# Kernel tuning notes

Hardware: AMD Instinct MI355X
Metric: run time of the kernel (lower is better)

Reference implementation:

```python
import jax, jax.numpy as jnp
import numpy as np
from jax import lax

VOCAB_SIZE = 13
E = 13          # embedding_dim == len(VOCAB)
H = 1024        # weights_dim (LSTM hidden)
HL = 512        # hidden_layer_dim (MLP)
OUT = 2
T = 16384       # sequence length


def setup_inputs() -> dict:
    key = jax.random.key(0)
    ks = jax.random.split(key, 12)
    s_ih = 1.0 / np.sqrt(H)  # PyTorch LSTMCell default init scale
    inp = {
        "x": jax.random.normal(ks[0], (T, E), dtype=jnp.float32),
        "h0": jax.random.normal(ks[1], (1, H), dtype=jnp.float32) * np.sqrt(2.0 / (1 + H)),
        "c0": jax.random.normal(ks[2], (1, H), dtype=jnp.float32) * np.sqrt(2.0 / (1 + H)),
        "W_ih": jax.random.uniform(ks[3], (4 * H, E), jnp.float32, -s_ih, s_ih),
        "W_hh": jax.random.uniform(ks[4], (4 * H, H), jnp.float32, -s_ih, s_ih),
        "b_ih": jax.random.uniform(ks[5], (4 * H,), jnp.float32, -s_ih, s_ih),
        "b_hh": jax.random.uniform(ks[6], (4 * H,), jnp.float32, -s_ih, s_ih),
        "W1": jax.random.uniform(ks[7], (HL, H), jnp.float32, -1.0 / np.sqrt(H), 1.0 / np.sqrt(H)),
        "b1": jax.random.uniform(ks[8], (HL,), jnp.float32, -1.0 / np.sqrt(H), 1.0 / np.sqrt(H)),
        "W2": jax.random.uniform(ks[9], (OUT, HL), jnp.float32, -1.0 / np.sqrt(HL), 1.0 / np.sqrt(HL)),
        "b2": jax.random.uniform(ks[10], (OUT,), jnp.float32, -1.0 / np.sqrt(HL), 1.0 / np.sqrt(HL)),
    }
    return inp


def reference(x, h0, c0, W_ih, W_hh, b_ih, b_hh, W1, b1, W2, b2):
    # x: [T, E] (batch dim of the original view is 1, folded away)
    # Precompute input-to-gate projections for all timesteps (same math, one GEMM).
    xg = x @ W_ih.T + b_ih  # [T, 4H]

    def step(carry, xg_t):
        h, c = carry  # [1, H] each
        gates = xg_t + h @ W_hh.T + b_hh  # [1, 4H]
        i, f, g, o = jnp.split(gates, 4, axis=-1)
        c = jax.nn.sigmoid(f) * c + jax.nn.sigmoid(i) * jnp.tanh(g)
        h = jax.nn.sigmoid(o) * jnp.tanh(c)
        return (h, c), None

    (h, c), _ = lax.scan(step, (h0, c0), xg[:, None, :])
    out = jnp.tanh(h @ W1.T + b1) @ W2.T + b2  # [1, 2]
    return out
```

## Files before the change

kernel.cpp:

```cpp
#include <hip/hip_runtime.h>
#include <cstdint>
#include <cstddef>

#define NWG 64
#define NTHR 512
#define UPW 16
#define TSTEPS 16384
#define HDIM 1024
#define EDIM 13
#define HLDIM 512

typedef unsigned long long ull;

__global__ void k_init(const float* __restrict__ h0, ull* __restrict__ hrec,
                       ull* __restrict__ urec) {
  int i = threadIdx.x;
  hrec[i] = (ull)__float_as_uint(h0[i]);
  hrec[HDIM + i] = 0ull;
  hrec[2 * HDIM + i] = 0ull;
  hrec[3 * HDIM + i] = 0ull;
  if (i < HLDIM) urec[i] = 0ull;
}

__global__ __launch_bounds__(NTHR) void k_main(
    const float* __restrict__ x, const float* __restrict__ c0,
    const float* __restrict__ Wih, const float* __restrict__ Whh,
    const float* __restrict__ bih, const float* __restrict__ bhh,
    const float* __restrict__ W1, const float* __restrict__ b1,
    const float* __restrict__ W2, const float* __restrict__ b2,
    float* __restrict__ out, ull* hrec, ull* urec) {
  const int w = blockIdx.x;
  const int tid = threadIdx.x;
  const int wave = tid >> 6;
  const int lane = tid & 63;
  const int hi = lane >> 5;
  const int sl = lane & 31;
  const int lu = 2 * wave + hi;

  __shared__ float4 lds_w4[32 * 256];
  __shared__ float4 lds_h4[2 * 256];
  __shared__ float lds_wih[64][17];
  __shared__ float lds_bsum[64];
  __shared__ float lds_r0[8], lds_r1[8];
  __shared__ float lds_xbuf[2][16];
  float* lds_hf = (float*)lds_h4;

#pragma unroll
  for (int it = 0; it < 16; ++it) {
    int idx = it * NTHR + tid;
    int r = idx >> 8;
    int c4 = idx & 255;
    int lu_ = r >> 2, g_ = r & 3;
    int grow = g_ * HDIM + UPW * w + lu_;
    lds_w4[r * 256 + c4] = ((const float4*)(Whh + (size_t)grow * HDIM))[c4];
  }
  if (tid < 64) {
    int lu_ = tid >> 2, g_ = tid & 3;
    int grow = g_ * HDIM + UPW * w + lu_;
#pragma unroll
    for (int e = 0; e < EDIM; ++e) lds_wih[tid][e] = Wih[grow * EDIM + e];
    lds_bsum[tid] = bih[grow] + bhh[grow];
  }
  float cst = c0[UPW * w + lu];
  __syncthreads();

  const int myg = sl & 3;
  const float gsc = (myg == 2) ? 2.f : 1.f;
  const float4* wl0 = lds_w4 + (size_t)(4 * lu + 0) * 256;
  const float4* wl1 = lds_w4 + (size_t)(4 * lu + 1) * 256;
  const float4* wl2 = lds_w4 + (size_t)(4 * lu + 2) * 256;
  const float4* wl3 = lds_w4 + (size_t)(4 * lu + 3) * 256;
  const float4* gg0 =
      (const float4*)(Whh + (size_t)(0 * HDIM + UPW * w + lu) * HDIM);
  const float4* gg1 =
      (const float4*)(Whh + (size_t)(1 * HDIM + UPW * w + lu) * HDIM);
  const float4* gg2 =
      (const float4*)(Whh + (size_t)(2 * HDIM + UPW * w + lu) * HDIM);
  const float4* gg3 =
      (const float4*)(Whh + (size_t)(3 * HDIM + UPW * w + lu) * HDIM);

  for (int t = 1; t <= TSTEPS; ++t) {
    const int lp = (t - 1) & 1;

    if (wave == 0) {
      float xv = 0.f;
      if (lane < EDIM) xv = x[(size_t)(t - 1) * EDIM + lane];

      const ull* src = hrec + (size_t)((t - 1) & 3) * HDIM;
      const unsigned want = (unsigned)(t - 1);
      ull v0, v1, v2, v3, v4, v5, v6, v7, v8, v9, va, vb, vc, vd, ve, vf;
      for (;;) {
        v0 = __hip_atomic_load(&src[lane], __ATOMIC_RELAXED,
                               __HIP_MEMORY_SCOPE_AGENT);
        v1 = __hip_atomic_load(&src[lane + 64], __ATOMIC_RELAXED,
                               __HIP_MEMORY_SCOPE_AGENT);
        v2 = __hip_atomic_load(&src[lane + 128], __ATOMIC_RELAXED,
                               __HIP_MEMORY_SCOPE_AGENT);
        v3 = __hip_atomic_load(&src[lane + 192], __ATOMIC_RELAXED,
                               __HIP_MEMORY_SCOPE_AGENT);
        v4 = __hip_atomic_load(&src[lane + 256], __ATOMIC_RELAXED,
                               __HIP_MEMORY_SCOPE_AGENT);
        v5 = __hip_atomic_load(&src[lane + 320], __ATOMIC_RELAXED,
                               __HIP_MEMORY_SCOPE_AGENT);
        v6 = __hip_atomic_load(&src[lane + 384], __ATOMIC_RELAXED,
                               __HIP_MEMORY_SCOPE_AGENT);
        v7 = __hip_atomic_load(&src[lane + 448], __ATOMIC_RELAXED,
                               __HIP_MEMORY_SCOPE_AGENT);
        v8 = __hip_atomic_load(&src[lane + 512], __ATOMIC_RELAXED,
                               __HIP_MEMORY_SCOPE_AGENT);
        v9 = __hip_atomic_load(&src[lane + 576], __ATOMIC_RELAXED,
                               __HIP_MEMORY_SCOPE_AGENT);
        va = __hip_atomic_load(&src[lane + 640], __ATOMIC_RELAXED,
                               __HIP_MEMORY_SCOPE_AGENT);
        vb = __hip_atomic_load(&src[lane + 704], __ATOMIC_RELAXED,
                               __HIP_MEMORY_SCOPE_AGENT);
        vc = __hip_atomic_load(&src[lane + 768], __ATOMIC_RELAXED,
                               __HIP_MEMORY_SCOPE_AGENT);
        vd = __hip_atomic_load(&src[lane + 832], __ATOMIC_RELAXED,
                               __HIP_MEMORY_SCOPE_AGENT);
        ve = __hip_atomic_load(&src[lane + 896], __ATOMIC_RELAXED,
                               __HIP_MEMORY_SCOPE_AGENT);
        vf = __hip_atomic_load(&src[lane + 960], __ATOMIC_RELAXED,
                               __HIP_MEMORY_SCOPE_AGENT);
        unsigned ok = ((unsigned)(v0 >> 32) == want) &
                      ((unsigned)(v1 >> 32) == want) &
                      ((unsigned)(v2 >> 32) == want) &
                      ((unsigned)(v3 >> 32) == want) &
                      ((unsigned)(v4 >> 32) == want) &
                      ((unsigned)(v5 >> 32) == want) &
                      ((unsigned)(v6 >> 32) == want) &
                      ((unsigned)(v7 >> 32) == want) &
                      ((unsigned)(v8 >> 32) == want) &
                      ((unsigned)(v9 >> 32) == want) &
                      ((unsigned)(va >> 32) == want) &
                      ((unsigned)(vb >> 32) == want) &
                      ((unsigned)(vc >> 32) == want) &
                      ((unsigned)(vd >> 32) == want) &
                      ((unsigned)(ve >> 32) == want) &
                      ((unsigned)(vf >> 32) == want);
        if (ok) break;
      }
      float* dst = lds_hf + lp * HDIM + lane;
      dst[0] = __uint_as_float((unsigned)v0);
      dst[64] = __uint_as_float((unsigned)v1);
      dst[128] = __uint_as_float((unsigned)v2);
      dst[192] = __uint_as_float((unsigned)v3);
      dst[256] = __uint_as_float((unsigned)v4);
      dst[320] = __uint_as_float((unsigned)v5);
      dst[384] = __uint_as_float((unsigned)v6);
      dst[448] = __uint_as_float((unsigned)v7);
      dst[512] = __uint_as_float((unsigned)v8);
      dst[576] = __uint_as_float((unsigned)v9);
      dst[640] = __uint_as_float((unsigned)va);
      dst[704] = __uint_as_float((unsigned)vb);
      dst[768] = __uint_as_float((unsigned)vc);
      dst[832] = __uint_as_float((unsigned)vd);
      dst[896] = __uint_as_float((unsigned)ve);
      dst[960] = __uint_as_float((unsigned)vf);
      if (lane < EDIM) lds_xbuf[lp][lane] = xv;
    }
    __syncthreads();

    const float4* hb = lds_h4 + lp * 256;
    float4 hv0 = hb[sl], hv1 = hb[sl + 32], hv2 = hb[sl + 64],
           hv3 = hb[sl + 96], hv4 = hb[sl + 128], hv5 = hb[sl + 160],
           hv6 = hb[sl + 192], hv7 = hb[sl + 224];

#define ROWDOT(dst, srcp)                                               \
  {                                                                     \
    float4 a = (srcp)[sl], b = (srcp)[sl + 32], c = (srcp)[sl + 64],    \
           d = (srcp)[sl + 96], e4 = (srcp)[sl + 128],                  \
           f4 = (srcp)[sl + 160], g4 = (srcp)[sl + 192],                \
           i4 = (srcp)[sl + 224];                                       \
    dst = (a.x * hv0.x + a.y * hv0.y + a.z * hv0.z + a.w * hv0.w) +     \
          (b.x * hv1.x + b.y * hv1.y + b.z * hv1.z + b.w * hv1.w) +     \
          (c.x * hv2.x + c.y * hv2.y + c.z * hv2.z + c.w * hv2.w) +     \
          (d.x * hv3.x + d.y * hv3.y + d.z * hv3.z + d.w * hv3.w) +     \
          (e4.x * hv4.x + e4.y * hv4.y + e4.z * hv4.z + e4.w * hv4.w) + \
          (f4.x * hv5.x + f4.y * hv5.y + f4.z * hv5.z + f4.w * hv5.w) + \
          (g4.x * hv6.x + g4.y * hv6.y + g4.z * hv6.z + g4.w * hv6.w) + \
          (i4.x * hv7.x + i4.y * hv7.y + i4.z * hv7.z + i4.w * hv7.w);  \
  }

    float acc0, acc1, acc2, acc3;
    if (lu < 8) {
      ROWDOT(acc0, wl0);
      ROWDOT(acc1, wl1);
      ROWDOT(acc2, wl2);
      ROWDOT(acc3, wl3);
    } else {
      ROWDOT(acc0, gg0);
      ROWDOT(acc1, gg1);
      ROWDOT(acc2, gg2);
      ROWDOT(acc3, gg3);
    }
#undef ROWDOT

    if (sl < 4) {
      int lrow = lu * 4 + sl;
      float xd = lds_bsum[lrow];
#pragma unroll
      for (int e = 0; e < EDIM; ++e) xd += lds_wih[lrow][e] * lds_xbuf[lp][e];
      if (sl == 0) acc0 += xd;
      else if (sl == 1) acc1 += xd;
      else if (sl == 2) acc2 += xd;
      else acc3 += xd;
    }

#pragma unroll
    for (int m = 1; m < 32; m <<= 1) {
      acc0 += __shfl_xor(acc0, m);
      acc1 += __shfl_xor(acc1, m);
      acc2 += __shfl_xor(acc2, m);
      acc3 += __shfl_xor(acc3, m);
    }

    float pre = (myg == 0) ? acc0 : (myg == 1) ? acc1 : (myg == 2) ? acc2
                                                                   : acc3;
    float e = __expf(-gsc * pre);
    float y = 1.f / (1.f + e);
    float act = (myg == 2) ? 2.f * y - 1.f : y;

    int base = lane & 32;
    float ai = __shfl(act, base + 0);
    float af = __shfl(act, base + 1);
    float ag = __shfl(act, base + 2);
    float ao = __shfl(act, base + 3);
    if (sl == 0) {
      cst = af * cst + ai * ag;
      float e2 = __expf(-2.f * cst);
      float hn = ao * (2.f / (1.f + e2) - 1.f);
      ull pk = ((ull)(unsigned)t << 32) | (ull)__float_as_uint(hn);
      __hip_atomic_store(&hrec[(size_t)(t & 3) * HDIM + UPW * w + lu], pk,
                         __ATOMIC_RELAXED, __HIP_MEMORY_SCOPE_AGENT);
    }
  }

  {
    const unsigned want = (unsigned)TSTEPS;
    ull v0 = __hip_atomic_load(&hrec[tid], __ATOMIC_RELAXED,
                               __HIP_MEMORY_SCOPE_AGENT);
    ull v1 = __hip_atomic_load(&hrec[tid + NTHR], __ATOMIC_RELAXED,
                               __HIP_MEMORY_SCOPE_AGENT);
    for (;;) {
      bool b0 = (unsigned)(v0 >> 32) == want;
      bool b1 = (unsigned)(v1 >> 32) == want;
      if (b0 && b1) break;
      if (!b0)
        v0 = __hip_atomic_load(&hrec[tid], __ATOMIC_RELAXED,
                               __HIP_MEMORY_SCOPE_AGENT);
      if (!b1)
        v1 = __hip_atomic_load(&hrec[tid + NTHR], __ATOMIC_RELAXED,
                               __HIP_MEMORY_SCOPE_AGENT);
    }
    lds_hf[tid] = __uint_as_float((unsigned)v0);
    lds_hf[tid + NTHR] = __uint_as_float((unsigned)v1);
  }
  __syncthreads();
  {
    int r1 = 8 * w + wave;
    const float* w1p = W1 + (size_t)r1 * HDIM + lane * 16;
    float a0 = 0.f, a1 = 0.f;
#pragma unroll
    for (int i = 0; i < 16; i += 2) {
      a0 += w1p[i] * lds_hf[lane * 16 + i];
      a1 += w1p[i + 1] * lds_hf[lane * 16 + i + 1];
    }
    float acc1 = a0 + a1;
#pragma unroll
    for (int m = 1; m < 64; m <<= 1) acc1 += __shfl_xor(acc1, m);
    if (lane == 0) {
      float e2 = __expf(-2.f * (acc1 + b1[r1]));
      float u = 2.f / (1.f + e2) - 1.f;
      ull pk = (1ull << 32) | (ull)__float_as_uint(u);
      __hip_atomic_store(&urec[r1], pk, __ATOMIC_RELAXED,
                         __HIP_MEMORY_SCOPE_AGENT);
    }
  }

  if (w == 0) {
    ull uv = __hip_atomic_load(&urec[tid], __ATOMIC_RELAXED,
                               __HIP_MEMORY_SCOPE_AGENT);
    while ((unsigned)(uv >> 32) != 1u)
      uv = __hip_atomic_load(&urec[tid], __ATOMIC_RELAXED,
                             __HIP_MEMORY_SCOPE_AGENT);
    float u = __uint_as_float((unsigned)uv);
    float p0 = W2[tid] * u;
    float p1 = W2[HLDIM + tid] * u;
#pragma unroll
    for (int m = 1; m < 64; m <<= 1) {
      p0 += __shfl_xor(p0, m);
      p1 += __shfl_xor(p1, m);
    }
    if (lane == 0) {
      lds_r0[wave] = p0;
      lds_r1[wave] = p1;
    }
    __syncthreads();
    if (tid == 0) {
      float o0 = b2[0], o1 = b2[1];
#pragma unroll
      for (int k = 0; k < 8; ++k) {
        o0 += lds_r0[k];
        o1 += lds_r1[k];
      }
      out[0] = o0;
      out[1] = o1;
    }
  }
}

extern "C" void kernel_launch(void* const* d_in, const int* in_sizes, int n_in,
                              void* d_out, int out_size, void* d_ws,
                              size_t ws_size, hipStream_t stream) {
  const float* x = (const float*)d_in[0];
  const float* h0 = (const float*)d_in[1];
  const float* c0 = (const float*)d_in[2];
  const float* Wih = (const float*)d_in[3];
  const float* Whh = (const float*)d_in[4];
  const float* bih = (const float*)d_in[5];
  const float* bhh = (const float*)d_in[6];
  const float* W1 = (const float*)d_in[7];
  const float* b1 = (const float*)d_in[8];
  const float* W2 = (const float*)d_in[9];
  const float* b2 = (const float*)d_in[10];
  float* out = (float*)d_out;

  ull* hrec = (ull*)d_ws;
  ull* urec = (ull*)((char*)d_ws + 4 * HDIM * sizeof(ull));

  k_init<<<1, 1024, 0, stream>>>(h0, hrec, urec);
  k_main<<<NWG, NTHR, 0, stream>>>(x, c0, Wih, Whh, bih, bhh, W1, b1, W2, b2,
                                   out, hrec, urec);
}
```

Measured before the change: 56.88 ms.

## Add two dedicated loader waves with LDS ready flags replacing per-step block barrier

The block grows from 8 to 10 waves. Two producer waves take turns polling the global h records for alternating timesteps and write h and x into a 4-deep LDS ring, then publish a per-slot ready flag. The 8 compute waves spin on that LDS flag instead of a __syncthreads, so the fetch of h for step t+1 can overlap compute of step t and the block-wide barrier leaves the critical path. The cost is extra waves, 4x more LDS for h, and volatile-flag spinning whose ordering rests on an explicit lgkmcnt wait.

```diff
diff --git a/kernel.cpp b/kernel.cpp
--- a/kernel.cpp
+++ b/kernel.cpp
@@ -3,7 +3,7 @@
 #include <cstddef>
 
 #define NWG 64
-#define NTHR 512
+#define NTHR 640
 #define UPW 16
 #define TSTEPS 16384
 #define HDIM 1024
@@ -35,24 +35,28 @@
   const int lane = tid & 63;
   const int hi = lane >> 5;
   const int sl = lane & 31;
-  const int lu = 2 * wave + hi;
+  const int cwave = wave - 2;
+  const int lu = (cwave >= 0) ? 2 * cwave + hi : 0;
 
   __shared__ float4 lds_w4[32 * 256];
-  __shared__ float4 lds_h4[2 * 256];
+  __shared__ float4 lds_h4[4 * 256];
   __shared__ float lds_wih[64][17];
   __shared__ float lds_bsum[64];
+  __shared__ float lds_xbuf[4][16];
   __shared__ float lds_r0[8], lds_r1[8];
-  __shared__ float lds_xbuf[2][16];
+  __shared__ int lds_rdy[4];
   float* lds_hf = (float*)lds_h4;
 
 #pragma unroll
-  for (int it = 0; it < 16; ++it) {
+  for (int it = 0; it < 13; ++it) {
     int idx = it * NTHR + tid;
-    int r = idx >> 8;
-    int c4 = idx & 255;
-    int lu_ = r >> 2, g_ = r & 3;
-    int grow = g_ * HDIM + UPW * w + lu_;
-    lds_w4[r * 256 + c4] = ((const float4*)(Whh + (size_t)grow * HDIM))[c4];
+    if (idx < 8192) {
+      int r = idx >> 8;
+      int c4 = idx & 255;
+      int lu_ = r >> 2, g_ = r & 3;
+      int grow = g_ * HDIM + UPW * w + lu_;
+      lds_w4[r * 256 + c4] = ((const float4*)(Whh + (size_t)grow * HDIM))[c4];
+    }
   }
   if (tid < 64) {
     int lu_ = tid >> 2, g_ = tid & 3;
@@ -61,86 +65,65 @@
     for (int e = 0; e < EDIM; ++e) lds_wih[tid][e] = Wih[grow * EDIM + e];
     lds_bsum[tid] = bih[grow] + bhh[grow];
   }
-  float cst = c0[UPW * w + lu];
+  if (tid < 4) lds_rdy[tid] = -1;
+  float cst = (cwave >= 0) ? c0[UPW * w + lu] : 0.f;
   __syncthreads();
 
-  const int myg = sl & 3;
-  const float gsc = (myg == 2) ? 2.f : 1.f;
-  const float4* wl0 = lds_w4 + (size_t)(4 * lu + 0) * 256;
-  const float4* wl1 = lds_w4 + (size_t)(4 * lu + 1) * 256;
-  const float4* wl2 = lds_w4 + (size_t)(4 * lu + 2) * 256;
-  const float4* wl3 = lds_w4 + (size_t)(4 * lu + 3) * 256;
-  const float4* gg0 =
-      (const float4*)(Whh + (size_t)(0 * HDIM + UPW * w + lu) * HDIM);
-  const float4* gg1 =
-      (const float4*)(Whh + (size_t)(1 * HDIM + UPW * w + lu) * HDIM);
-  const float4* gg2 =
-      (const float4*)(Whh + (size_t)(2 * HDIM + UPW * w + lu) * HDIM);
-  const float4* gg3 =
-      (const float4*)(Whh + (size_t)(3 * HDIM + UPW * w + lu) * HDIM);
-
-  for (int t = 1; t <= TSTEPS; ++t) {
-    const int lp = (t - 1) & 1;
-
-    if (wave == 0) {
+  if (wave < 2) {
+    for (int t = 1 + wave; t <= TSTEPS; t += 2) {
+      const int p = (t - 1) & 3;
       float xv = 0.f;
       if (lane < EDIM) xv = x[(size_t)(t - 1) * EDIM + lane];
 
-      const ull* src = hrec + (size_t)((t - 1) & 3) * HDIM;
+      const ull* src = hrec + (size_t)p * HDIM + lane;
       const unsigned want = (unsigned)(t - 1);
       ull v0, v1, v2, v3, v4, v5, v6, v7, v8, v9, va, vb, vc, vd, ve, vf;
       for (;;) {
-        v0 = __hip_atomic_load(&src[lane], __ATOMIC_RELAXED,
-                               __HIP_MEMORY_SCOPE_AGENT);
-        v1 = __hip_atomic_load(&src[lane + 64], __ATOMIC_RELAXED,
-                               __HIP_MEMORY_SCOPE_AGENT);
-        v2 = __hip_atomic_load(&src[lane + 128], __ATOMIC_RELAXED,
-                               __HIP_MEMORY_SCOPE_AGENT);
-        v3 = __hip_atomic_load(&src[lane + 192], __ATOMIC_RELAXED,
-                               __HIP_MEMORY_SCOPE_AGENT);
-        v4 = __hip_atomic_load(&src[lane + 256], __ATOMIC_RELAXED,
-                               __HIP_MEMORY_SCOPE_AGENT);
-        v5 = __hip_atomic_load(&src[lane + 320], __ATOMIC_RELAXED,
-                               __HIP_MEMORY_SCOPE_AGENT);
-        v6 = __hip_atomic_load(&src[lane + 384], __ATOMIC_RELAXED,
-                               __HIP_MEMORY_SCOPE_AGENT);
-        v7 = __hip_atomic_load(&src[lane + 448], __ATOMIC_RELAXED,
-                               __HIP_MEMORY_SCOPE_AGENT);
-        v8 = __hip_atomic_load(&src[lane + 512], __ATOMIC_RELAXED,
-                               __HIP_MEMORY_SCOPE_AGENT);
-        v9 = __hip_atomic_load(&src[lane + 576], __ATOMIC_RELAXED,
-                               __HIP_MEMORY_SCOPE_AGENT);
-        va = __hip_atomic_load(&src[lane + 640], __ATOMIC_RELAXED,
-                               __HIP_MEMORY_SCOPE_AGENT);
-        vb = __hip_atomic_load(&src[lane + 704], __ATOMIC_RELAXED,
-                               __HIP_MEMORY_SCOPE_AGENT);
-        vc = __hip_atomic_load(&src[lane + 768], __ATOMIC_RELAXED,
-                               __HIP_MEMORY_SCOPE_AGENT);
-        vd = __hip_atomic_load(&src[lane + 832], __ATOMIC_RELAXED,
-                               __HIP_MEMORY_SCOPE_AGENT);
-        ve = __hip_atomic_load(&src[lane + 896], __ATOMIC_RELAXED,
-                               __HIP_MEMORY_SCOPE_AGENT);
-        vf = __hip_atomic_load(&src[lane + 960], __ATOMIC_RELAXED,
-                               __HIP_MEMORY_SCOPE_AGENT);
-        unsigned ok = ((unsigned)(v0 >> 32) == want) &
-                      ((unsigned)(v1 >> 32) == want) &
-                      ((unsigned)(v2 >> 32) == want) &
-                      ((unsigned)(v3 >> 32) == want) &
-                      ((unsigned)(v4 >> 32) == want) &
-                      ((unsigned)(v5 >> 32) == want) &
-                      ((unsigned)(v6 >> 32) == want) &
-                      ((unsigned)(v7 >> 32) == want) &
-                      ((unsigned)(v8 >> 32) == want) &
-                      ((unsigned)(v9 >> 32) == want) &
-                      ((unsigned)(va >> 32) == want) &
-                      ((unsigned)(vb >> 32) == want) &
-                      ((unsigned)(vc >> 32) == want) &
-                      ((unsigned)(vd >> 32) == want) &
-                      ((unsigned)(ve >> 32) == want) &
-                      ((unsigned)(vf >> 32) == want);
+        v0 = __hip_atomic_load(&src[0], __ATOMIC_RELAXED,
+                               __HIP_MEMORY_SCOPE_AGENT);
+        v1 = __hip_atomic_load(&src[64], __ATOMIC_RELAXED,
+                               __HIP_MEMORY_SCOPE_AGENT);
+        v2 = __hip_atomic_load(&src[128], __ATOMIC_RELAXED,
+                               __HIP_MEMORY_SCOPE_AGENT);
+        v3 = __hip_atomic_load(&src[192], __ATOMIC_RELAXED,
+                               __HIP_MEMORY_SCOPE_AGENT);
+        v4 = __hip_atomic_load(&src[256], __ATOMIC_RELAXED,
+                               __HIP_MEMORY_SCOPE_AGENT);
+        v5 = __hip_atomic_load(&src[320], __ATOMIC_RELAXED,
+                               __HIP_MEMORY_SCOPE_AGENT);
+        v6 = __hip_atomic_load(&src[384], __ATOMIC_RELAXED,
+                               __HIP_MEMORY_SCOPE_AGENT);
+        v7 = __hip_atomic_load(&src[448], __ATOMIC_RELAXED,
+                               __HIP_MEMORY_SCOPE_AGENT);
+        v8 = __hip_atomic_load(&src[512], __ATOMIC_RELAXED,
+                               __HIP_MEMORY_SCOPE_AGENT);
+        v9 = __hip_atomic_load(&src[576], __ATOMIC_RELAXED,
+                               __HIP_MEMORY_SCOPE_AGENT);
+        va = __hip_atomic_load(&src[640], __ATOMIC_RELAXED,
+                               __HIP_MEMORY_SCOPE_AGENT);
+        vb = __hip_atomic_load(&src[704], __ATOMIC_RELAXED,
+                               __HIP_MEMORY_SCOPE_AGENT);
+        vc = __hip_atomic_load(&src[768], __ATOMIC_RELAXED,
+                               __HIP_MEMORY_SCOPE_AGENT);
+        vd = __hip_atomic_load(&src[832], __ATOMIC_RELAXED,
+                               __HIP_MEMORY_SCOPE_AGENT);
+        ve = __hip_atomic_load(&src[896], __ATOMIC_RELAXED,
+                               __HIP_MEMORY_SCOPE_AGENT);
+        vf = __hip_atomic_load(&src[960], __ATOMIC_RELAXED,
+                               __HIP_MEMORY_SCOPE_AGENT);
+        unsigned ok =
+            ((unsigned)(v0 >> 32) == want) & ((unsigned)(v1 >> 32) == want) &
+            ((unsigned)(v2 >> 32) == want) & ((unsigned)(v3 >> 32) == want) &
+            ((unsigned)(v4 >> 32) == want) & ((unsigned)(v5 >> 32) == want) &
+            ((unsigned)(v6 >> 32) == want) & ((unsigned)(v7 >> 32) == want) &
+            ((unsigned)(v8 >> 32) == want) & ((unsigned)(v9 >> 32) == want) &
+            ((unsigned)(va >> 32) == want) & ((unsigned)(vb >> 32) == want) &
+            ((unsigned)(vc >> 32) == want) & ((unsigned)(vd >> 32) == want) &
+            ((unsigned)(ve >> 32) == want) & ((unsigned)(vf >> 32) == want);
         if (ok) break;
       }
-      float* dst = lds_hf + lp * HDIM + lane;
+      if (lane < EDIM) lds_xbuf[p][lane] = xv;
+      float* dst = lds_hf + p * HDIM + lane;
       dst[0] = __uint_as_float((unsigned)v0);
       dst[64] = __uint_as_float((unsigned)v1);
       dst[128] = __uint_as_float((unsigned)v2);
@@ -157,14 +140,35 @@
       dst[832] = __uint_as_float((unsigned)vd);
       dst[896] = __uint_as_float((unsigned)ve);
       dst[960] = __uint_as_float((unsigned)vf);
-      if (lane < EDIM) lds_xbuf[lp][lane] = xv;
-    }
-    __syncthreads();
-
-    const float4* hb = lds_h4 + lp * 256;
-    float4 hv0 = hb[sl], hv1 = hb[sl + 32], hv2 = hb[sl + 64],
-           hv3 = hb[sl + 96], hv4 = hb[sl + 128], hv5 = hb[sl + 160],
-           hv6 = hb[sl + 192], hv7 = hb[sl + 224];
+      asm volatile("s_waitcnt lgkmcnt(0)" ::: "memory");
+      if (lane == 0) ((volatile int*)lds_rdy)[p] = t - 1;
+    }
+  } else {
+    const int myg = sl & 3;
+    const float gsc = (myg == 2) ? 2.f : 1.f;
+    const float4* wl0 = lds_w4 + (size_t)(4 * lu + 0) * 256;
+    const float4* wl1 = lds_w4 + (size_t)(4 * lu + 1) * 256;
+    const float4* wl2 = lds_w4 + (size_t)(4 * lu + 2) * 256;
+    const float4* wl3 = lds_w4 + (size_t)(4 * lu + 3) * 256;
+    const float4* gg0 =
+        (const float4*)(Whh + (size_t)(0 * HDIM + UPW * w + lu) * HDIM);
+    const float4* gg1 =
+        (const float4*)(Whh + (size_t)(1 * HDIM + UPW * w + lu) * HDIM);
+    const float4* gg2 =
+        (const float4*)(Whh + (size_t)(2 * HDIM + UPW * w + lu) * HDIM);
+    const float4* gg3 =
+        (const float4*)(Whh + (size_t)(3 * HDIM + UPW * w + lu) * HDIM);
+
+    for (int t = 1; t <= TSTEPS; ++t) {
+      const int p = (t - 1) & 3;
+      volatile int* rp = (volatile int*)lds_rdy + p;
+      while (*rp != t - 1) {
+      }
+
+      const float4* hb = lds_h4 + p * 256;
+      float4 hv0 = hb[sl], hv1 = hb[sl + 32], hv2 = hb[sl + 64],
+             hv3 = hb[sl + 96], hv4 = hb[sl + 128], hv5 = hb[sl + 160],
+             hv6 = hb[sl + 192], hv7 = hb[sl + 224];
 
 #define ROWDOT(dst, srcp)                                               \
   {                                                                     \
@@ -182,65 +186,67 @@
           (i4.x * hv7.x + i4.y * hv7.y + i4.z * hv7.z + i4.w * hv7.w);  \
   }
 
-    float acc0, acc1, acc2, acc3;
-    if (lu < 8) {
-      ROWDOT(acc0, wl0);
-      ROWDOT(acc1, wl1);
-      ROWDOT(acc2, wl2);
-      ROWDOT(acc3, wl3);
-    } else {
-      ROWDOT(acc0, gg0);
-      ROWDOT(acc1, gg1);
-      ROWDOT(acc2, gg2);
-      ROWDOT(acc3, gg3);
-    }
+      float acc0, acc1, acc2, acc3;
+      if (lu < 8) {
+        ROWDOT(acc0, wl0);
+        ROWDOT(acc1, wl1);
+        ROWDOT(acc2, wl2);
+        ROWDOT(acc3, wl3);
+      } else {
+        ROWDOT(acc0, gg0);
+        ROWDOT(acc1, gg1);
+        ROWDOT(acc2, gg2);
+        ROWDOT(acc3, gg3);
+      }
 #undef ROWDOT
 
-    if (sl < 4) {
-      int lrow = lu * 4 + sl;
-      float xd = lds_bsum[lrow];
-#pragma unroll
-      for (int e = 0; e < EDIM; ++e) xd += lds_wih[lrow][e] * lds_xbuf[lp][e];
-      if (sl == 0) acc0 += xd;
-      else if (sl == 1) acc1 += xd;
-      else if (sl == 2) acc2 += xd;
-      else acc3 += xd;
-    }
-
-#pragma unroll
-    for (int m = 1; m < 32; m <<= 1) {
-      acc0 += __shfl_xor(acc0, m);
-      acc1 += __shfl_xor(acc1, m);
-      acc2 += __shfl_xor(acc2, m);
-      acc3 += __shfl_xor(acc3, m);
-    }
-
-    float pre = (myg == 0) ? acc0 : (myg == 1) ? acc1 : (myg == 2) ? acc2
-                                                                   : acc3;
-    float e = __expf(-gsc * pre);
-    float y = 1.f / (1.f + e);
-    float act = (myg == 2) ? 2.f * y - 1.f : y;
-
-    int base = lane & 32;
-    float ai = __shfl(act, base + 0);
-    float af = __shfl(act, base + 1);
-    float ag = __shfl(act, base + 2);
-    float ao = __shfl(act, base + 3);
-    if (sl == 0) {
-      cst = af * cst + ai * ag;
-      float e2 = __expf(-2.f * cst);
-      float hn = ao * (2.f / (1.f + e2) - 1.f);
-      ull pk = ((ull)(unsigned)t << 32) | (ull)__float_as_uint(hn);
-      __hip_atomic_store(&hrec[(size_t)(t & 3) * HDIM + UPW * w + lu], pk,
-                         __ATOMIC_RELAXED, __HIP_MEMORY_SCOPE_AGENT);
-    }
-  }
-
-  {
+      if (sl < 4) {
+        int lrow = lu * 4 + sl;
+        float xd = lds_bsum[lrow];
+#pragma unroll
+        for (int e = 0; e < EDIM; ++e) xd += lds_wih[lrow][e] * lds_xbuf[p][e];
+        if (sl == 0) acc0 += xd;
+        else if (sl == 1) acc1 += xd;
+        else if (sl == 2) acc2 += xd;
+        else acc3 += xd;
+      }
+
+#pragma unroll
+      for (int m = 1; m < 32; m <<= 1) {
+        acc0 += __shfl_xor(acc0, m);
+        acc1 += __shfl_xor(acc1, m);
+        acc2 += __shfl_xor(acc2, m);
+        acc3 += __shfl_xor(acc3, m);
+      }
+
+      float pre = (myg == 0) ? acc0 : (myg == 1) ? acc1 : (myg == 2) ? acc2
+                                                                     : acc3;
+      float e = __expf(-gsc * pre);
+      float y = 1.f / (1.f + e);
+      float act = (myg == 2) ? 2.f * y - 1.f : y;
+
+      int base = lane & 32;
+      float ai = __shfl(act, base + 0);
+      float af = __shfl(act, base + 1);
+      float ag = __shfl(act, base + 2);
+      float ao = __shfl(act, base + 3);
+      if (sl == 0) {
+        cst = af * cst + ai * ag;
+        float e2 = __expf(-2.f * cst);
+        float hn = ao * (2.f / (1.f + e2) - 1.f);
+        ull pk = ((ull)(unsigned)t << 32) | (ull)__float_as_uint(hn);
+        __hip_atomic_store(&hrec[(size_t)(t & 3) * HDIM + UPW * w + lu], pk,
+                           __ATOMIC_RELAXED, __HIP_MEMORY_SCOPE_AGENT);
+      }
+    }
+  }
+
+  __syncthreads();
+  if (tid < 512) {
     const unsigned want = (unsigned)TSTEPS;
     ull v0 = __hip_atomic_load(&hrec[tid], __ATOMIC_RELAXED,
                                __HIP_MEMORY_SCOPE_AGENT);
-    ull v1 = __hip_atomic_load(&hrec[tid + NTHR], __ATOMIC_RELAXED,
+    ull v1 = __hip_atomic_load(&hrec[tid + 512], __ATOMIC_RELAXED,
                                __HIP_MEMORY_SCOPE_AGENT);
     for (;;) {
       bool b0 = (unsigned)(v0 >> 32) == want;
@@ -250,14 +256,14 @@
         v0 = __hip_atomic_load(&hrec[tid], __ATOMIC_RELAXED,
                                __HIP_MEMORY_SCOPE_AGENT);
       if (!b1)
-        v1 = __hip_atomic_load(&hrec[tid + NTHR], __ATOMIC_RELAXED,
+        v1 = __hip_atomic_load(&hrec[tid + 512], __ATOMIC_RELAXED,
                                __HIP_MEMORY_SCOPE_AGENT);
     }
     lds_hf[tid] = __uint_as_float((unsigned)v0);
-    lds_hf[tid + NTHR] = __uint_as_float((unsigned)v1);
+    lds_hf[tid + 512] = __uint_as_float((unsigned)v1);
   }
   __syncthreads();
-  {
+  if (wave < 8) {
     int r1 = 8 * w + wave;
     const float* w1p = W1 + (size_t)r1 * HDIM + lane * 16;
     float a0 = 0.f, a1 = 0.f;
@@ -279,20 +285,23 @@
   }
 
   if (w == 0) {
-    ull uv = __hip_atomic_load(&urec[tid], __ATOMIC_RELAXED,
-                               __HIP_MEMORY_SCOPE_AGENT);
-    while ((unsigned)(uv >> 32) != 1u)
-      uv = __hip_atomic_load(&urec[tid], __ATOMIC_RELAXED,
-                             __HIP_MEMORY_SCOPE_AGENT);
-    float u = __uint_as_float((unsigned)uv);
-    float p0 = W2[tid] * u;
-    float p1 = W2[HLDIM + tid] * u;
+    float p0 = 0.f, p1 = 0.f;
+    if (tid < HLDIM) {
+      ull uv = __hip_atomic_load(&urec[tid], __ATOMIC_RELAXED,
+                                 __HIP_MEMORY_SCOPE_AGENT);
+      while ((unsigned)(uv >> 32) != 1u)
+        uv = __hip_atomic_load(&urec[tid], __ATOMIC_RELAXED,
+                               __HIP_MEMORY_SCOPE_AGENT);
+      float u = __uint_as_float((unsigned)uv);
+      p0 = W2[tid] * u;
+      p1 = W2[HLDIM + tid] * u;
+    }
 #pragma unroll
     for (int m = 1; m < 64; m <<= 1) {
       p0 += __shfl_xor(p0, m);
       p1 += __shfl_xor(p1, m);
     }
-    if (lane == 0) {
+    if (lane == 0 && wave < 8) {
       lds_r0[wave] = p0;
       lds_r1[wave] = p1;
     }
```

Result: slower. 102.1 ms (+79.5%).
